# Kernel optimization log

Measured on AMD Instinct MI355X. Metric: run time of the kernel, lower is better.

The kernel has to match this reference:

```python
import jax, jax.numpy as jnp
import numpy as np

N = 100_000   # nodes
E = 3_200_000 # edges (avg degree 32)

def _glorot(k, shape):
    fan_in, fan_out = shape
    lim = float(np.sqrt(6.0 / (fan_in + fan_out)))
    return jax.random.uniform(k, shape, jnp.float32, -lim, lim)

def setup_inputs() -> dict:
    key = jax.random.key(0)
    ks = jax.random.split(key, 8)
    x = jax.random.normal(ks[0], (N, 3), dtype=jnp.float32)
    edge_index = jax.random.randint(ks[1], (2, E), 0, N, dtype=jnp.int32)
    choices = jax.random.bernoulli(ks[2], 0.5, (N,))
    W1 = _glorot(ks[3], (3, 16));  b1 = jnp.zeros((16,), jnp.float32)
    W2 = _glorot(ks[4], (16, 16)); b2 = jnp.zeros((16,), jnp.float32)
    W3 = _glorot(ks[5], (16, 1));  b3 = jnp.zeros((1,), jnp.float32)
    fc_w = _glorot(ks[6], (16, 1)); fc_b = jnp.zeros((1,), jnp.float32)
    return dict(x=x, edge_index=edge_index, choices=choices,
                W1=W1, b1=b1, W2=W2, b2=b2, W3=W3, b3=b3,
                fc_w=fc_w, fc_b=fc_b)

def reference(x, edge_index, choices, W1, b1, W2, b2, W3, b3, fc_w, fc_b):
    row, col = edge_index[0], edge_index[1]  # source -> target
    # improved=True GCN norm: self-loop weight 2, deg = in_degree + 2
    deg = jax.ops.segment_sum(jnp.ones((E,), x.dtype), col, num_segments=N) + 2.0
    dinv = jax.lax.rsqrt(deg)                    # [N]
    enorm = dinv[row] * dinv[col]                # [E] edge normalization
    self_norm = 2.0 * dinv * dinv                # [N] self-loop term

    def gcn(h, W, b):
        h = h @ W                                # [N, F_out]
        agg = jax.ops.segment_sum(h[row] * enorm[:, None], col, num_segments=N)
        return agg + self_norm[:, None] * h + b

    h = jax.nn.relu(gcn(x, W1, b1))
    h = jax.nn.relu(gcn(h, W2, b2))
    c = gcn(h, W3, b3)[:, 0]                     # [N] per-node logit
    # masked softmax over chosen nodes (torch masked_select + softmax,
    # expressed with static shape: non-chosen entries get probability 0)
    logits = jnp.where(choices, c, -jnp.inf)
    choice = jax.nn.softmax(logits, axis=0)      # [N]
    # global_mean_pool with a single graph = mean over all nodes
    v = jnp.mean(h, axis=0, keepdims=True)       # [1, 16]
    value = v @ fc_w + fc_b                      # [1, 1]
    return choice, value
```

## Files before the change

### kernel.cpp

```cpp
#include <hip/hip_runtime.h>
#include <hip/hip_fp16.h>
#include <math.h>

#define BLK 256


#define BSH 7
#define NBK 128
#define NB 1024
#define CAP 5120
#define SCAP 6144
#define EB 8192
#define BINTH 1024

__device__ inline float4 load_h4(const __half* base, int node, int sub) {
    const uint2* p = reinterpret_cast<const uint2*>(base + ((size_t)node << 4)) + sub;
    uint2 u = *p;
    union { unsigned u; __half2 h; } a, b;
    a.u = u.x; b.u = u.y;
    float2 fa = __half22float2(a.h), fb = __half22float2(b.h);
    return make_float4(fa.x, fa.y, fb.x, fb.y);
}

__device__ inline void store_h4(__half* base, int node, int sub, float4 v) {
    union { unsigned u; __half2 h; } a, b;
    a.h = __floats2half2_rn(v.x, v.y);
    b.h = __floats2half2_rn(v.z, v.w);
    uint2 u; u.x = a.u; u.y = b.u;
    *(reinterpret_cast<uint2*>(base + ((size_t)node << 4)) + sub) = u;
}

__device__ inline float3 load_xs(const __half* xs, int node) {
    uint2 u = *reinterpret_cast<const uint2*>(xs + ((size_t)node << 2));
    union { unsigned u; __half2 h; } a, b;
    a.u = u.x; b.u = u.y;
    float2 fa = __half22float2(a.h), fb = __half22float2(b.h);
    return make_float3(fa.x, fa.y, fb.x);
}

__global__ void k_init(int* __restrict__ gcur, float* __restrict__ scal) {
    int t = threadIdx.x;
    gcur[t] = 0;
    if (t < 18) scal[t] = 0.f;
}

__global__ void __launch_bounds__(BINTH) k_bin(const int* __restrict__ row,
                                               const int* __restrict__ col,
                                               int* __restrict__ gcur,
                                               int* __restrict__ packed, int E) {
    __shared__ int stage[EB];
    __shared__ unsigned short sbuk[EB];
    __shared__ int hist[NB];
    __shared__ int lscan[NB];
    __shared__ int cur[NB];
    __shared__ int gbase[NB];
    int tid = threadIdx.x;
    int base = blockIdx.x * EB;
    int cnt = min(EB, E - base);

    hist[tid] = 0;
    __syncthreads();
    for (int j = tid; j < cnt; j += BINTH) {
        int c = __builtin_nontemporal_load(col + base + j);
        atomicAdd(&hist[c >> BSH], 1);
    }
    __syncthreads();
    lscan[tid] = hist[tid];
    __syncthreads();
    for (int d = 1; d < NB; d <<= 1) {
        int t = (tid >= d) ? lscan[tid - d] : 0;
        __syncthreads();
        if (tid >= d) lscan[tid] += t;
        __syncthreads();
    }
    {
        int ex = lscan[tid] - hist[tid];
        lscan[tid] = ex;
        cur[tid] = ex;
    }
    __syncthreads();
    for (int j = tid; j < cnt; j += BINTH) {
        int c = __builtin_nontemporal_load(col + base + j);
        int r = __builtin_nontemporal_load(row + base + j);
        int b = c >> BSH;
        int p = atomicAdd(&cur[b], 1);
        stage[p] = (r << BSH) | (c & ((1 << BSH) - 1));
        sbuk[p] = (unsigned short)b;
    }
    __syncthreads();
    if (hist[tid] > 0)
        gbase[tid] = tid * CAP + atomicAdd(&gcur[tid], hist[tid]);
    __syncthreads();
    for (int j = tid; j < cnt; j += BINTH) {
        int b = sbuk[j];
        int pos = gbase[b] + (j - lscan[b]);
        packed[pos] = stage[j];
    }
}

__global__ void __launch_bounds__(BLK) k_place(const int* __restrict__ packed,
                                               const int* __restrict__ bcnt,
                                               const float* __restrict__ x,
                                               int* __restrict__ degi,
                                               int* __restrict__ offs,
                                               float* __restrict__ dinv,
                                               __half* __restrict__ xs,
                                               int* __restrict__ srcs, int n) {
    __shared__ int cnt[NBK];
    __shared__ int lcur[NBK];
    __shared__ int ssum[NBK];
    __shared__ int stg[SCAP];
    int tid = threadIdx.x;
    int b = blockIdx.x;
    int nb0 = b << BSH;
    if (tid < NBK) cnt[tid] = 0;
    __syncthreads();
    int ecnt = bcnt[b];
    const int* pk = packed + (size_t)b * CAP;
    for (int j = tid; j < ecnt; j += BLK)
        atomicAdd(&cnt[pk[j] & (NBK - 1)], 1);
    __syncthreads();
    int c = 0, pl = 0;
    if (tid < NBK) {
        c = cnt[tid];
        pl = (c + 7) & ~7;
        ssum[tid] = pl;
    }
    __syncthreads();
    for (int d = 1; d < NBK; d <<= 1) {
        int t = (tid < NBK && tid >= d) ? ssum[tid - d] : 0;
        __syncthreads();
        if (tid < NBK && tid >= d) ssum[tid] += t;
        __syncthreads();
    }
    int valid = min(n - nb0, NBK);
    int i = nb0 + tid;
    if (tid < NBK) {
        int Arel = ssum[tid] - pl;
        lcur[tid] = Arel;
        int A = b * SCAP + Arel;
        if (tid < valid) {
            degi[i] = pl;
            offs[i] = A;
            float di = rsqrtf((float)c + 2.0f);
            dinv[i] = di;
            float x0 = x[i * 3 + 0], x1 = x[i * 3 + 1], x2 = x[i * 3 + 2];
            union { unsigned u; __half2 h; } a2, b2u;
            a2.h = __floats2half2_rn(di * x0, di * x1);
            b2u.h = __floats2half2_rn(di * x2, 0.f);
            uint2 u; u.x = a2.u; u.y = b2u.u;
            *reinterpret_cast<uint2*>(xs + ((size_t)i << 2)) = u;
            for (int k = c; k < pl; k++) stg[Arel + k] = n;
        }
    }
    if (b == 0 && tid == 0) {
        uint2 z; z.x = 0u; z.y = 0u;
        *reinterpret_cast<uint2*>(xs + ((size_t)n << 2)) = z;
    }
    __syncthreads();
    for (int j = tid; j < ecnt; j += BLK) {
        int v = pk[j];
        int slot = atomicAdd(&lcur[v & (NBK - 1)], 1);
        stg[slot] = v >> BSH;
    }
    __syncthreads();
    int total = ssum[NBK - 1];
    int gb = b * SCAP;
    for (int j = tid; j < total; j += BLK)
        srcs[gb + j] = stg[j];
}

__global__ void __launch_bounds__(BLK) k_agg1(const __half* __restrict__ xs,
                                              const int* __restrict__ offs,
                                              const int* __restrict__ degi,
                                              const int* __restrict__ srcs,
                                              const float* __restrict__ dinv,
                                              const float* __restrict__ b1,
                                              const float* __restrict__ W1,
                                              const float* __restrict__ W2,
                                              __half* __restrict__ hwsB, int n) {
    __shared__ float w1[48];
    __shared__ float w2[256];
    __shared__ float bb[16];
    __shared__ float hbuf[64][17];
    int tid = threadIdx.x;
    w2[tid] = W2[tid];
    if (tid < 48) w1[tid] = W1[tid];
    if (tid < 16) bb[tid] = b1[tid];
    if (blockIdx.x == 0 && tid < 8)
        reinterpret_cast<unsigned*>(hwsB + ((size_t)n << 4))[tid] = 0u;
    __syncthreads();
    int t = tid >> 2, sub = tid & 3;
    int i = blockIdx.x * 64 + t;
    bool act = (i < n);
    int A  = act ? offs[i] : 0;
    int pl = act ? degi[i] : 0;
    int o = 4 * sub;
    int clamp = max(pl - 4, 0);
    float ax0 = 0.f, ay0 = 0.f, az0 = 0.f;
    float ax1 = 0.f, ay1 = 0.f, az1 = 0.f;
    for (int j = 0; j < pl; j += 32) {
        int i0 = j + o;
        int i1 = j + 16 + o;
        int ja = min(i0, clamp);
        int jb = min(i1, clamp);
        int4 sa = *reinterpret_cast<const int4*>(srcs + A + ja);
        int4 sb = *reinterpret_cast<const int4*>(srcs + A + jb);
        if (i0 >= pl) sa = make_int4(n, n, n, n);
        if (i1 >= pl) sb = make_int4(n, n, n, n);
        float3 qa0 = load_xs(xs, sa.x);
        float3 qa1 = load_xs(xs, sa.y);
        float3 qa2 = load_xs(xs, sa.z);
        float3 qa3 = load_xs(xs, sa.w);
        float3 qb0 = load_xs(xs, sb.x);
        float3 qb1 = load_xs(xs, sb.y);
        float3 qb2 = load_xs(xs, sb.z);
        float3 qb3 = load_xs(xs, sb.w);
        ax0 += qa0.x + qa1.x + qa2.x + qa3.x;
        ay0 += qa0.y + qa1.y + qa2.y + qa3.y;
        az0 += qa0.z + qa1.z + qa2.z + qa3.z;
        ax1 += qb0.x + qb1.x + qb2.x + qb3.x;
        ay1 += qb0.y + qb1.y + qb2.y + qb3.y;
        az1 += qb0.z + qb1.z + qb2.z + qb3.z;
    }
    float ax = ax0 + ax1, ay = ay0 + ay1, az = az0 + az1;
    ax += __shfl_xor(ax, 1); ay += __shfl_xor(ay, 1); az += __shfl_xor(az, 1);
    ax += __shfl_xor(ax, 2); ay += __shfl_xor(ay, 2); az += __shfl_xor(az, 2);
    float di = 0.f;
    if (act) {
        di = dinv[i];
        float3 s = load_xs(xs, i);
        float axs = ax + 2.f * s.x, ays = ay + 2.f * s.y, azs = az + 2.f * s.z;
#pragma unroll
        for (int k = 0; k < 4; k++) {
            int f = sub * 4 + k;
            float hv = di * (axs * w1[f] + ays * w1[16 + f] + azs * w1[32 + f]) + bb[f];
            hbuf[t][f] = fmaxf(hv, 0.f);
        }
    }
    __syncthreads();
    if (act) {
        const float* hn = hbuf[t];
        float s0 = 0.f, s1 = 0.f, s2 = 0.f, s3 = 0.f;
#pragma unroll
        for (int f = 0; f < 16; f++) {
            float hv = hn[f];
            const float4 wq = *(const float4*)&w2[f * 16 + sub * 4];
            s0 += hv * wq.x; s1 += hv * wq.y; s2 += hv * wq.z; s3 += hv * wq.w;
        }
        store_h4(hwsB, i, sub, make_float4(di * s0, di * s1, di * s2, di * s3));
    }
}

__global__ void __launch_bounds__(BLK) k_agg2(const __half* __restrict__ hwsB,
                                              const int* __restrict__ offs,
                                              const int* __restrict__ degi,
                                              const int* __restrict__ srcs,
                                              const float* __restrict__ dinv,
                                              const float* __restrict__ b2,
                                              const float* __restrict__ W3,
                                              float* __restrict__ hws3,
                                              float* __restrict__ pool, int n) {
    __shared__ float w3[16];
    __shared__ float bb[16];
    __shared__ float lp[16];
    int tid = threadIdx.x;
    if (tid < 16) { w3[tid] = W3[tid]; bb[tid] = b2[tid]; lp[tid] = 0.f; }
    if (blockIdx.x == 0 && tid == 0) hws3[n] = 0.f;
    __syncthreads();
    int t = tid >> 2, sub = tid & 3;
    int i = blockIdx.x * 64 + t;
    bool act = (i < n);
    float di = act ? dinv[i] : 0.f;
    int A  = act ? offs[i] : 0;
    int pl = act ? degi[i] : 0;
    float4 z4 = make_float4(0.f, 0.f, 0.f, 0.f);
    float4 s = act ? load_h4(hwsB, i, sub) : z4;
    float4 acc0 = make_float4(2.f * s.x, 2.f * s.y, 2.f * s.z, 2.f * s.w);
    float4 acc1 = z4, acc2 = z4, acc3 = z4;
    int clamp8 = max(pl - 8, 0);
    for (int j = 0; j < pl; j += 16) {
        int j1 = j + 8;
        int jb = min(j1, clamp8);
        int4 sa0 = *reinterpret_cast<const int4*>(srcs + A + j);
        int4 sa1 = *reinterpret_cast<const int4*>(srcs + A + j + 4);
        int4 sb0 = *reinterpret_cast<const int4*>(srcs + A + jb);
        int4 sb1 = *reinterpret_cast<const int4*>(srcs + A + jb + 4);
        if (j1 >= pl) { sb0 = make_int4(n, n, n, n); sb1 = sb0; }
        float4 qa0 = load_h4(hwsB, sa0.x, sub);
        float4 qa1 = load_h4(hwsB, sa0.y, sub);
        float4 qa2 = load_h4(hwsB, sa0.z, sub);
        float4 qa3 = load_h4(hwsB, sa0.w, sub);
        float4 qa4 = load_h4(hwsB, sa1.x, sub);
        float4 qa5 = load_h4(hwsB, sa1.y, sub);
        float4 qa6 = load_h4(hwsB, sa1.z, sub);
        float4 qa7 = load_h4(hwsB, sa1.w, sub);
        float4 qb0 = load_h4(hwsB, sb0.x, sub);
        float4 qb1 = load_h4(hwsB, sb0.y, sub);
        float4 qb2 = load_h4(hwsB, sb0.z, sub);
        float4 qb3 = load_h4(hwsB, sb0.w, sub);
        float4 qb4 = load_h4(hwsB, sb1.x, sub);
        float4 qb5 = load_h4(hwsB, sb1.y, sub);
        float4 qb6 = load_h4(hwsB, sb1.z, sub);
        float4 qb7 = load_h4(hwsB, sb1.w, sub);
        acc0.x += qa0.x + qa2.x + qa4.x + qa6.x;
        acc0.y += qa0.y + qa2.y + qa4.y + qa6.y;
        acc0.z += qa0.z + qa2.z + qa4.z + qa6.z;
        acc0.w += qa0.w + qa2.w + qa4.w + qa6.w;
        acc1.x += qa1.x + qa3.x + qa5.x + qa7.x;
        acc1.y += qa1.y + qa3.y + qa5.y + qa7.y;
        acc1.z += qa1.z + qa3.z + qa5.z + qa7.z;
        acc1.w += qa1.w + qa3.w + qa5.w + qa7.w;
        acc2.x += qb0.x + qb2.x + qb4.x + qb6.x;
        acc2.y += qb0.y + qb2.y + qb4.y + qb6.y;
        acc2.z += qb0.z + qb2.z + qb4.z + qb6.z;
        acc2.w += qb0.w + qb2.w + qb4.w + qb6.w;
        acc3.x += qb1.x + qb3.x + qb5.x + qb7.x;
        acc3.y += qb1.y + qb3.y + qb5.y + qb7.y;
        acc3.z += qb1.z + qb3.z + qb5.z + qb7.z;
        acc3.w += qb1.w + qb3.w + qb5.w + qb7.w;
    }
    acc0.x += acc1.x + acc2.x + acc3.x;
    acc0.y += acc1.y + acc2.y + acc3.y;
    acc0.z += acc1.z + acc2.z + acc3.z;
    acc0.w += acc1.w + acc2.w + acc3.w;
    float4 hA = z4;
    if (act) {
        hA.x = fmaxf(di * acc0.x + bb[sub * 4 + 0], 0.f);
        hA.y = fmaxf(di * acc0.y + bb[sub * 4 + 1], 0.f);
        hA.z = fmaxf(di * acc0.z + bb[sub * 4 + 2], 0.f);
        hA.w = fmaxf(di * acc0.w + bb[sub * 4 + 3], 0.f);
    }
    float pA = hA.x * w3[sub * 4 + 0] + hA.y * w3[sub * 4 + 1]
             + hA.z * w3[sub * 4 + 2] + hA.w * w3[sub * 4 + 3];
    pA += __shfl_xor(pA, 1); pA += __shfl_xor(pA, 2);
    if (sub == 0 && act) hws3[i] = di * pA;
    float4 hp = hA;
#pragma unroll
    for (int m = 4; m < 64; m <<= 1) {
        hp.x += __shfl_xor(hp.x, m);
        hp.y += __shfl_xor(hp.y, m);
        hp.z += __shfl_xor(hp.z, m);
        hp.w += __shfl_xor(hp.w, m);
    }
    if ((tid & 63) < 4) {
        atomicAdd(&lp[sub * 4 + 0], hp.x);
        atomicAdd(&lp[sub * 4 + 1], hp.y);
        atomicAdd(&lp[sub * 4 + 2], hp.z);
        atomicAdd(&lp[sub * 4 + 3], hp.w);
    }
    __syncthreads();
    if (tid < 16) atomicAdd(&pool[tid], lp[tid]);
}

__global__ void __launch_bounds__(BLK) k_agg3(const float* __restrict__ hws3,
                                              const int* __restrict__ offs,
                                              const int* __restrict__ degi,
                                              const int* __restrict__ srcs,
                                              const float* __restrict__ dinv,
                                              const float* __restrict__ b3,
                                              const int* __restrict__ choices,
                                              float* __restrict__ cbuf,
                                              float* __restrict__ bmax,
                                              float* __restrict__ bsum, int n) {
    __shared__ float red[BLK];
    int tid = threadIdx.x;
    int nl = tid >> 2, sub = tid & 3;
    int iA = blockIdx.x * 128 + nl;
    int iB = iA + 64;
    bool actA = (iA < n), actB = (iB < n);
    int AA = actA ? offs[iA] : 0;
    int AB = actB ? offs[iB] : 0;
    int plA = actA ? degi[iA] : 0;
    int plB = actB ? degi[iB] : 0;
    float sA0 = 0.f, sA1 = 0.f, sB0 = 0.f, sB1 = 0.f;
    int plM = max(plA, plB);
    for (int j = 8 * sub; j < plM; j += 32) {
        int ja = min(j, max(plA - 8, 0));
        int jb = min(j, max(plB - 8, 0));
        int4 sa0 = *reinterpret_cast<const int4*>(srcs + AA + ja);
        int4 sa1 = *reinterpret_cast<const int4*>(srcs + AA + ja + 4);
        int4 sb0 = *reinterpret_cast<const int4*>(srcs + AB + jb);
        int4 sb1 = *reinterpret_cast<const int4*>(srcs + AB + jb + 4);
        if (j >= plA) { sa0 = make_int4(n, n, n, n); sa1 = sa0; }
        if (j >= plB) { sb0 = make_int4(n, n, n, n); sb1 = sb0; }
        sA0 += hws3[sa0.x] + hws3[sa0.z] + hws3[sa1.x] + hws3[sa1.z];
        sA1 += hws3[sa0.y] + hws3[sa0.w] + hws3[sa1.y] + hws3[sa1.w];
        sB0 += hws3[sb0.x] + hws3[sb0.z] + hws3[sb1.x] + hws3[sb1.z];
        sB1 += hws3[sb0.y] + hws3[sb0.w] + hws3[sb1.y] + hws3[sb1.w];
    }
    float sA = sA0 + sA1, sB = sB0 + sB1;
    sA += __shfl_xor(sA, 1); sA += __shfl_xor(sA, 2);
    sB += __shfl_xor(sB, 1); sB += __shfl_xor(sB, 2);
    float lA = -INFINITY, lB = -INFINITY;
    if (sub == 0) {
        if (actA) {
            float c = dinv[iA] * (sA + 2.f * hws3[iA]) + b3[0];
            cbuf[iA] = c;
            if (choices[iA] != 0) lA = c;
        }
        if (actB) {
            float c = dinv[iB] * (sB + 2.f * hws3[iB]) + b3[0];
            cbuf[iB] = c;
            if (choices[iB] != 0) lB = c;
        }
    }
    red[tid] = fmaxf(lA, lB);
    __syncthreads();
    for (int d = BLK / 2; d > 0; d >>= 1) {
        if (tid < d) red[tid] = fmaxf(red[tid], red[tid + d]);
        __syncthreads();
    }
    float bm = red[0];
    __syncthreads();
    float es = 0.f;
    if (lA > -INFINITY) es += expf(lA - bm);
    if (lB > -INFINITY) es += expf(lB - bm);
    red[tid] = es;
    __syncthreads();
    for (int d = BLK / 2; d > 0; d >>= 1) {
        if (tid < d) red[tid] += red[tid + d];
        __syncthreads();
    }
    if (tid == 0) { bmax[blockIdx.x] = bm; bsum[blockIdx.x] = red[0]; }
}

__global__ void __launch_bounds__(BLK) k_final(const float* __restrict__ cbuf,
                                               const int* __restrict__ choices,
                                               const float* __restrict__ bmax,
                                               const float* __restrict__ bsum,
                                               const float* __restrict__ pool,
                                               const float* __restrict__ fcw,
                                               const float* __restrict__ fcb,
                                               float* __restrict__ out,
                                               int nblk, int n) {
    __shared__ float red[BLK];
    __shared__ float MS[2];
    int tid = threadIdx.x;
    float m = -INFINITY;
    for (int i = tid; i < nblk; i += BLK) m = fmaxf(m, bmax[i]);
    red[tid] = m;
    __syncthreads();
    for (int d = BLK / 2; d > 0; d >>= 1) {
        if (tid < d) red[tid] = fmaxf(red[tid], red[tid + d]);
        __syncthreads();
    }
    float M = red[0];
    __syncthreads();
    float s = 0.f;
    for (int i = tid; i < nblk; i += BLK) {
        float bm = bmax[i];
        if (bm > -INFINITY) s += bsum[i] * expf(bm - M);
    }
    red[tid] = s;
    __syncthreads();
    for (int d = BLK / 2; d > 0; d >>= 1) {
        if (tid < d) red[tid] += red[tid + d];
        __syncthreads();
    }
    if (tid == 0) { MS[0] = M; MS[1] = red[0]; }
    __syncthreads();
    float Mv = MS[0], Sv = MS[1];
    int i = blockIdx.x * BLK + tid;
    if (i < n) {
        float p = 0.0f;
        if (choices[i] != 0) p = expf(cbuf[i] - Mv) / Sv;
        out[i] = p;
    }
    if (blockIdx.x == 0 && tid == 0) {
        float invn = 1.0f / (float)n;
        float v = 0.0f;
#pragma unroll
        for (int f = 0; f < 16; f++) v += (pool[f] * invn) * fcw[f];
        out[n] = v + fcb[0];
    }
}

extern "C" void kernel_launch(void* const* d_in, const int* in_sizes, int n_in,
                              void* d_out, int out_size, void* d_ws, size_t ws_size,
                              hipStream_t stream) {
    const float* x       = (const float*)d_in[0];
    const int*   ei      = (const int*)d_in[1];
    const int*   choices = (const int*)d_in[2];
    const float* W1 = (const float*)d_in[3];
    const float* b1 = (const float*)d_in[4];
    const float* W2 = (const float*)d_in[5];
    const float* b2 = (const float*)d_in[6];
    const float* W3 = (const float*)d_in[7];
    const float* b3 = (const float*)d_in[8];
    const float* fcw = (const float*)d_in[9];
    const float* fcb = (const float*)d_in[10];
    float* out = (float*)d_out;

    int n = in_sizes[0] / 3;
    int E = in_sizes[1] / 2;
    const int* row = ei;
    const int* col = ei + E;

    int nblkN = (n + BLK - 1) / BLK;
    int nblk64 = (n + 63) / 64;
    int nblk128 = (n + 127) / 128;
    int nbuck = (n + NBK - 1) >> BSH;
    int nblkBin = (E + EB - 1) / EB;

    char* ws = (char*)d_ws;
    size_t o = 0;
    auto alloc = [&](size_t bytes) { char* p = ws + o; o += (bytes + 15) & ~(size_t)15; return p; };
    int*   degi   = (int*)  alloc((size_t)n * 4);
    int*   offs   = (int*)  alloc((size_t)n * 4);
    float* dinv   = (float*)alloc((size_t)n * 4);
    float* hws3   = (float*)alloc((size_t)(n + 1) * 4);
    float* cbuf   = (float*)alloc((size_t)n * 4);
    float* bmax   = (float*)alloc(8192);
    float* bsum   = (float*)alloc(8192);
    int*   gcur   = (int*)  alloc(NB * 4);
    float* scal   = (float*)alloc(256);
    float* pool   = scal + 1;
    __half* xs    = (__half*)alloc((size_t)(n + 1) * 4 * 2);
    size_t hw_bytes = (size_t)(n + 1) * 16 * 2;
    size_t pk_bytes = (size_t)NB * CAP * 4;
    char*  blob   = alloc(hw_bytes > pk_bytes ? hw_bytes : pk_bytes);
    int*    packed = (int*)blob;
    __half* hwsB   = (__half*)blob;
    int*   srcs   = (int*)  alloc((size_t)NB * SCAP * 4);
    (void)ws_size;

    k_init<<<1, NB, 0, stream>>>(gcur, scal);
    k_bin<<<nblkBin, BINTH, 0, stream>>>(row, col, gcur, packed, E);
    k_place<<<nbuck, BLK, 0, stream>>>(packed, gcur, x, degi, offs, dinv, xs, srcs, n);

    k_agg1<<<nblk64, BLK, 0, stream>>>(xs, offs, degi, srcs, dinv, b1, W1, W2, hwsB, n);
    k_agg2<<<nblk64, BLK, 0, stream>>>(hwsB, offs, degi, srcs, dinv, b2, W3, hws3, pool, n);
    k_agg3<<<nblk128, BLK, 0, stream>>>(hws3, offs, degi, srcs, dinv, b3, choices, cbuf, bmax, bsum, n);

    k_final<<<nblkN, BLK, 0, stream>>>(cbuf, choices, bmax, bsum, pool, fcw, fcb, out, nblk128, n);
}
```

Before: 211.2 us.

## Use wavefront shuffle scans in binning kernels and halve edges per bin block

Replaces the shared-memory Hillis-Steele prefix scans in k_bin and k_place with wave-level __shfl_up scans plus a small cross-wave combine, cutting the scan's many __syncthreads barriers to two. It also halves the edges handled per k_bin block, doubling the block count and shrinking shared memory per block, which may raise occupancy. The trade-off is more global atomics on bucket cursors and more per-block histogram and scan overhead.

```diff
diff --git a/kernel.cpp b/kernel.cpp
--- a/kernel.cpp
+++ b/kernel.cpp
@@ -10,7 +10,7 @@
 #define NB 1024
 #define CAP 5120
 #define SCAP 6144
-#define EB 8192
+#define EB 4096
 #define BINTH 1024
 
 __device__ inline float4 load_h4(const __half* base, int node, int sub) {
@@ -54,6 +54,7 @@
     __shared__ int lscan[NB];
     __shared__ int cur[NB];
     __shared__ int gbase[NB];
+    __shared__ int wpart[16];
     int tid = threadIdx.x;
     int base = blockIdx.x * EB;
     int cnt = min(EB, E - base);
@@ -65,19 +66,30 @@
         atomicAdd(&hist[c >> BSH], 1);
     }
     __syncthreads();
-    lscan[tid] = hist[tid];
-    __syncthreads();
-    for (int d = 1; d < NB; d <<= 1) {
-        int t = (tid >= d) ? lscan[tid - d] : 0;
-        __syncthreads();
-        if (tid >= d) lscan[tid] += t;
-        __syncthreads();
-    }
-    {
-        int ex = lscan[tid] - hist[tid];
-        lscan[tid] = ex;
-        cur[tid] = ex;
-    }
+    int lane = tid & 63, wid = tid >> 6;
+    int v = hist[tid];
+    int s = v;
+#pragma unroll
+    for (int d = 1; d < 64; d <<= 1) {
+        int t = __shfl_up(s, d);
+        if (lane >= d) s += t;
+    }
+    if (lane == 63) wpart[wid] = s;
+    __syncthreads();
+    if (wid == 0 && lane < 16) {
+        int w = wpart[lane];
+        int ss = w;
+#pragma unroll
+        for (int d = 1; d < 16; d <<= 1) {
+            int t = __shfl_up(ss, d);
+            if (lane >= d) ss += t;
+        }
+        wpart[lane] = ss - w;
+    }
+    __syncthreads();
+    int ex = s + wpart[wid] - v;
+    lscan[tid] = ex;
+    cur[tid] = ex;
     __syncthreads();
     for (int j = tid; j < cnt; j += BINTH) {
         int c = __builtin_nontemporal_load(col + base + j);
@@ -109,6 +121,7 @@
     __shared__ int cnt[NBK];
     __shared__ int lcur[NBK];
     __shared__ int ssum[NBK];
+    __shared__ int wp2[2];
     __shared__ int stg[SCAP];
     int tid = threadIdx.x;
     int b = blockIdx.x;
@@ -120,23 +133,26 @@
     for (int j = tid; j < ecnt; j += BLK)
         atomicAdd(&cnt[pk[j] & (NBK - 1)], 1);
     __syncthreads();
+    int lane = tid & 63, wid = tid >> 6;
     int c = 0, pl = 0;
     if (tid < NBK) {
         c = cnt[tid];
         pl = (c + 7) & ~7;
-        ssum[tid] = pl;
-    }
-    __syncthreads();
-    for (int d = 1; d < NBK; d <<= 1) {
-        int t = (tid < NBK && tid >= d) ? ssum[tid - d] : 0;
-        __syncthreads();
-        if (tid < NBK && tid >= d) ssum[tid] += t;
-        __syncthreads();
-    }
+    }
+    int s = pl;
+#pragma unroll
+    for (int d = 1; d < 64; d <<= 1) {
+        int t = __shfl_up(s, d);
+        if (lane >= d) s += t;
+    }
+    if (tid < NBK && lane == 63) wp2[wid] = s;
+    __syncthreads();
+    int incl = s + ((tid < NBK && wid == 1) ? wp2[0] : 0);
+    if (tid < NBK) ssum[tid] = incl;
     int valid = min(n - nb0, NBK);
     int i = nb0 + tid;
     if (tid < NBK) {
-        int Arel = ssum[tid] - pl;
+        int Arel = incl - pl;
         lcur[tid] = Arel;
         int A = b * SCAP + Arel;
         if (tid < valid) {
```

New measurement: 217.5 us. 3.0% more time.
